# Kernel optimization log

Measured on AMD Instinct MI355X. Metric: run time of the kernel, lower is better.

Reference implementation:

```python
import jax, jax.numpy as jnp
import numpy as np

THRESH = 0.9   # config['thresh_cnn']
R = 2          # config['radius'] -> maxpool kernel 2R+1=5, stride 1, padding R


def setup_inputs() -> dict:
    key = jax.random.key(0)
    # [B=1, C=1, D=64, H=512, W=512]
    pred_vol = jax.random.uniform(key, (1, 1, 64, 512, 512), dtype=jnp.float32)
    return {"pred_vol": pred_vol}


def reference(pred_vol):
    # threshold: keep values > thresh, else 0
    pred_thresh = jnp.where(pred_vol > THRESH, pred_vol, 0.0)
    # 3D max-pool, kernel 2R+1, stride 1, padding R (torch pads with -inf for maxpool)
    k = 2 * R + 1
    mp = jax.lax.reduce_window(
        pred_thresh, -jnp.inf, jax.lax.max,
        window_dimensions=(1, 1, k, k, k),
        window_strides=(1, 1, 1, 1, 1),
        padding=[(0, 0), (0, 0), (R, R), (R, R), (R, R)],
    )
    # keep only strict local maxima of the thresholded volume
    conf_vol = jnp.where((mp > 0.0) & (mp == pred_thresh), mp, 0.0)
    return jnp.squeeze(conf_vol)  # [D, H, W] dense peak confidence map
```

## Files before the change

### kernel.cpp

```cpp
#include <hip/hip_runtime.h>


#define THRESH 0.9f

constexpr int D = 64, H = 512, W = 512;
constexpr int TW = 64;
constexpr int TH = 16;
constexpr int DCHUNK = 8;
constexpr int HALO = 2;
constexpr int LROWS = TH + 2 * HALO;
constexpr int RAWQ  = TW / 4 + 2;
constexpr int RAWQ_S = RAWQ + 1;
constexpr int WMQ   = TW / 4;
constexpr int WMQ_S = WMQ + 1;
constexpr int NS = DCHUNK + 2 * HALO;
constexpr int T_ITERS = NS + 1;

typedef float floatx4 __attribute__((ext_vector_type(4)));

__device__ __forceinline__ float4 thresh4(float4 v) {
    v.x = (v.x > THRESH) ? v.x : 0.f;
    v.y = (v.y > THRESH) ? v.y : 0.f;
    v.z = (v.z > THRESH) ? v.z : 0.f;
    v.w = (v.w > THRESH) ? v.w : 0.f;
    return v;
}

__device__ __forceinline__ float4 max4(float4 a, float4 b) {
    return make_float4(fmaxf(a.x, b.x), fmaxf(a.y, b.y),
                       fmaxf(a.z, b.z), fmaxf(a.w, b.w));
}

__device__ __forceinline__ float4 wmax5(float4 a, float4 b, float4 c) {
    const float f2 = a.z, f3 = a.w, f4 = b.x, f5 = b.y, f6 = b.z, f7 = b.w;
    const float f8 = c.x, f9 = c.y;
    const float m45 = fmaxf(f4, f5);
    const float m56 = fmaxf(f5, f6);
    const float m345 = fmaxf(f3, m45);
    const float m456 = fmaxf(f4, m56);
    const float m567 = fmaxf(m56, f7);
    const float m678 = fmaxf(fmaxf(f6, f7), f8);
    float4 r;
    r.x = fmaxf(fmaxf(f2, f6), m345);
    r.y = fmaxf(fmaxf(f3, f7), m456);
    r.z = fmaxf(fmaxf(f4, f8), m567);
    r.w = fmaxf(fmaxf(f5, f9), m678);
    return r;
}

__global__ __launch_bounds__(256)
void peak3d_kernel(const float* __restrict__ in, float* __restrict__ out) {
    __shared__ float4 raw[2][LROWS * RAWQ_S];
    __shared__ float4 wm [2][LROWS * WMQ_S];

    const int tx = threadIdx.x;
    const int ty = threadIdx.y;
    const int tid = ty * 16 + tx;

    const int w0 = blockIdx.x * TW;
    const int h0 = blockIdx.y * TH;
    const int d0 = blockIdx.z * DCHUNK;

    const int q0 = tid;
    const int q1 = tid + 256;
    const int r0 = q0 / RAWQ, c0 = q0 % RAWQ;
    const int r1 = q1 / RAWQ, c1 = q1 % RAWQ;
    const int lds0 = r0 * RAWQ_S + c0;
    const int lds1 = r1 * RAWQ_S + c1;
    const int gh0 = h0 + r0 - HALO, gw0 = w0 + 4 * c0 - 4;
    const int gh1 = h0 + r1 - HALO, gw1 = w0 + 4 * c1 - 4;
    const bool has1 = (q1 < LROWS * RAWQ);
    const bool ib0 = (gh0 >= 0 && gh0 < H && gw0 >= 0 && gw0 < W);
    const bool ib1 = has1 && (gh1 >= 0 && gh1 < H && gw1 >= 0 && gw1 < W);
    const size_t off0 = ib0 ? ((size_t)gh0 * W + gw0) : 0;
    const size_t off1 = ib1 ? ((size_t)gh1 * W + gw1) : 0;

    const float4 zero4 = make_float4(0.f, 0.f, 0.f, 0.f);
    float4 win[5], cen[5];
#pragma unroll
    for (int k = 0; k < 5; ++k) { win[k] = zero4; cen[k] = zero4; }

    auto loadSlice = [&](int dd, float4& p0, float4& p1) {
        p0 = zero4; p1 = zero4;
        if (dd >= 0 && dd < D) {
            const size_t base = (size_t)dd * (H * W);
            if (ib0) p0 = thresh4(*reinterpret_cast<const float4*>(in + base + off0));
            if (ib1) p1 = thresh4(*reinterpret_cast<const float4*>(in + base + off1));
        }
    };

    float4 p0, p1;
    loadSlice(d0 - HALO, p0, p1);

    for (int jj = 0; jj < (T_ITERS + 4) / 5; ++jj) {
#pragma unroll
        for (int k = 0; k < 5; ++k) {
            const int t = 5 * jj + k;
            if (t < T_ITERS) {
                const int buf = t & 1;

                if (t <= NS - 1) {
                    raw[buf][lds0] = p0;
                    if (has1) raw[buf][lds1] = p1;
                }
                if (t + 1 <= NS - 1) loadSlice(d0 - HALO + t + 1, p0, p1);

                __syncthreads();

                if (t <= NS - 1) {
                    const float4* rp = &raw[buf][ty * RAWQ_S + tx];
                    wm[buf][ty * WMQ_S + tx] = wmax5(rp[0], rp[1], rp[2]);
                    if (tid < (LROWS - TH) * WMQ) {
                        const int r = TH + (tid >> 4), c = tid & 15;
                        const float4* rq = &raw[buf][r * RAWQ_S + c];
                        wm[buf][r * WMQ_S + c] = wmax5(rq[0], rq[1], rq[2]);
                    }
                    cen[k] = raw[buf][(ty + HALO) * RAWQ_S + (tx + 1)];
                }

                if (t >= 1) {
                    const float4* wp = &wm[buf ^ 1][ty * WMQ_S + tx];
                    float4 hv = wp[0];
                    hv = max4(hv, wp[1 * WMQ_S]);
                    hv = max4(hv, wp[2 * WMQ_S]);
                    hv = max4(hv, wp[3 * WMQ_S]);
                    hv = max4(hv, wp[4 * WMQ_S]);
                    win[(k + 4) % 5] = hv;

                    if (t >= 5) {
                        const int dout = d0 + (t - 5);
                        const float4 mp = max4(max4(max4(win[0], win[1]),
                                                    max4(win[2], win[3])), win[4]);
                        const float4 tcc = cen[(k + 2) % 5];
                        floatx4 res;
                        res.x = (mp.x > 0.f && mp.x == tcc.x) ? mp.x : 0.f;
                        res.y = (mp.y > 0.f && mp.y == tcc.y) ? mp.y : 0.f;
                        res.z = (mp.z > 0.f && mp.z == tcc.z) ? mp.z : 0.f;
                        res.w = (mp.w > 0.f && mp.w == tcc.w) ? mp.w : 0.f;
                        floatx4* op = reinterpret_cast<floatx4*>(
                            out + (size_t)dout * (H * W) +
                            (size_t)(h0 + ty) * W + (w0 + 4 * tx));
                        __builtin_nontemporal_store(res, op);
                    }
                }
            }
        }
    }
}

extern "C" void kernel_launch(void* const* d_in, const int* in_sizes, int n_in,
                              void* d_out, int out_size, void* d_ws, size_t ws_size,
                              hipStream_t stream) {
    const float* in = (const float*)d_in[0];
    float* out = (float*)d_out;
    dim3 grid(W / TW, H / TH, D / DCHUNK);
    dim3 block(16, 16, 1);
    hipLaunchKernelGGL(peak3d_kernel, grid, block, 0, stream, in, out);
}
```

Baseline: 122.1 us.

## Prefetch two depth slices ahead and use LDS-only barriers with single-buffered LDS

Restructures the depth-streaming loop so global loads for slice t+2 are issued two iterations ahead in alternating register slots. Replaces __syncthreads with an inline-asm barrier that waits only on LDS counters (lgkmcnt), so outstanding global loads and nontemporal stores are not drained at each barrier. The double-buffered LDS becomes single-buffered, with two barriers per slice and a fully unrolled loop. The aim is to hide memory latency better, at the cost of an extra barrier per iteration and more registers held for prefetch.

```diff
diff --git a/kernel.cpp b/kernel.cpp
--- a/kernel.cpp
+++ b/kernel.cpp
@@ -14,9 +14,12 @@
 constexpr int WMQ   = TW / 4;
 constexpr int WMQ_S = WMQ + 1;
 constexpr int NS = DCHUNK + 2 * HALO;
-constexpr int T_ITERS = NS + 1;
 
 typedef float floatx4 __attribute__((ext_vector_type(4)));
+
+__device__ __forceinline__ void barrier_no_drain() {
+    asm volatile("s_waitcnt lgkmcnt(0)\n\ts_barrier" ::: "memory");
+}
 
 __device__ __forceinline__ float4 thresh4(float4 v) {
     v.x = (v.x > THRESH) ? v.x : 0.f;
@@ -50,8 +53,8 @@
 
 __global__ __launch_bounds__(256)
 void peak3d_kernel(const float* __restrict__ in, float* __restrict__ out) {
-    __shared__ float4 raw[2][LROWS * RAWQ_S];
-    __shared__ float4 wm [2][LROWS * WMQ_S];
+    __shared__ float4 raw[LROWS * RAWQ_S];
+    __shared__ float4 wm [LROWS * WMQ_S];
 
     const int tx = threadIdx.x;
     const int ty = threadIdx.y;
@@ -80,69 +83,65 @@
 #pragma unroll
     for (int k = 0; k < 5; ++k) { win[k] = zero4; cen[k] = zero4; }
 
-    auto loadSlice = [&](int dd, float4& p0, float4& p1) {
-        p0 = zero4; p1 = zero4;
+    auto loadSlice = [&](int dd, float4& a, float4& b) {
+        a = zero4; b = zero4;
         if (dd >= 0 && dd < D) {
             const size_t base = (size_t)dd * (H * W);
-            if (ib0) p0 = thresh4(*reinterpret_cast<const float4*>(in + base + off0));
-            if (ib1) p1 = thresh4(*reinterpret_cast<const float4*>(in + base + off1));
+            if (ib0) a = thresh4(*reinterpret_cast<const float4*>(in + base + off0));
+            if (ib1) b = thresh4(*reinterpret_cast<const float4*>(in + base + off1));
         }
     };
 
-    float4 p0, p1;
-    loadSlice(d0 - HALO, p0, p1);
+    float4 pfa[2], pfb[2];
+    loadSlice(d0 - HALO + 0, pfa[0], pfb[0]);
+    loadSlice(d0 - HALO + 1, pfa[1], pfb[1]);
 
-    for (int jj = 0; jj < (T_ITERS + 4) / 5; ++jj) {
 #pragma unroll
-        for (int k = 0; k < 5; ++k) {
-            const int t = 5 * jj + k;
-            if (t < T_ITERS) {
-                const int buf = t & 1;
+    for (int t = 0; t < NS; ++t) {
+        const int slot = t & 1;
 
-                if (t <= NS - 1) {
-                    raw[buf][lds0] = p0;
-                    if (has1) raw[buf][lds1] = p1;
-                }
-                if (t + 1 <= NS - 1) loadSlice(d0 - HALO + t + 1, p0, p1);
+        raw[lds0] = pfa[slot];
+        if (has1) raw[lds1] = pfb[slot];
+        if (t + 2 < NS) loadSlice(d0 - HALO + t + 2, pfa[slot], pfb[slot]);
 
-                __syncthreads();
+        barrier_no_drain();
 
-                if (t <= NS - 1) {
-                    const float4* rp = &raw[buf][ty * RAWQ_S + tx];
-                    wm[buf][ty * WMQ_S + tx] = wmax5(rp[0], rp[1], rp[2]);
-                    if (tid < (LROWS - TH) * WMQ) {
-                        const int r = TH + (tid >> 4), c = tid & 15;
-                        const float4* rq = &raw[buf][r * RAWQ_S + c];
-                        wm[buf][r * WMQ_S + c] = wmax5(rq[0], rq[1], rq[2]);
-                    }
-                    cen[k] = raw[buf][(ty + HALO) * RAWQ_S + (tx + 1)];
-                }
+        {
+            const float4* rp = &raw[ty * RAWQ_S + tx];
+            wm[ty * WMQ_S + tx] = wmax5(rp[0], rp[1], rp[2]);
+            if (tid < (LROWS - TH) * WMQ) {
+                const int r = TH + (tid >> 4), c = tid & 15;
+                const float4* rq = &raw[r * RAWQ_S + c];
+                wm[r * WMQ_S + c] = wmax5(rq[0], rq[1], rq[2]);
+            }
+            cen[t % 5] = raw[(ty + HALO) * RAWQ_S + (tx + 1)];
+        }
 
-                if (t >= 1) {
-                    const float4* wp = &wm[buf ^ 1][ty * WMQ_S + tx];
-                    float4 hv = wp[0];
-                    hv = max4(hv, wp[1 * WMQ_S]);
-                    hv = max4(hv, wp[2 * WMQ_S]);
-                    hv = max4(hv, wp[3 * WMQ_S]);
-                    hv = max4(hv, wp[4 * WMQ_S]);
-                    win[(k + 4) % 5] = hv;
+        barrier_no_drain();
 
-                    if (t >= 5) {
-                        const int dout = d0 + (t - 5);
-                        const float4 mp = max4(max4(max4(win[0], win[1]),
-                                                    max4(win[2], win[3])), win[4]);
-                        const float4 tcc = cen[(k + 2) % 5];
-                        floatx4 res;
-                        res.x = (mp.x > 0.f && mp.x == tcc.x) ? mp.x : 0.f;
-                        res.y = (mp.y > 0.f && mp.y == tcc.y) ? mp.y : 0.f;
-                        res.z = (mp.z > 0.f && mp.z == tcc.z) ? mp.z : 0.f;
-                        res.w = (mp.w > 0.f && mp.w == tcc.w) ? mp.w : 0.f;
-                        floatx4* op = reinterpret_cast<floatx4*>(
-                            out + (size_t)dout * (H * W) +
-                            (size_t)(h0 + ty) * W + (w0 + 4 * tx));
-                        __builtin_nontemporal_store(res, op);
-                    }
-                }
+        {
+            const float4* wp = &wm[ty * WMQ_S + tx];
+            float4 hv = wp[0];
+            hv = max4(hv, wp[1 * WMQ_S]);
+            hv = max4(hv, wp[2 * WMQ_S]);
+            hv = max4(hv, wp[3 * WMQ_S]);
+            hv = max4(hv, wp[4 * WMQ_S]);
+            win[t % 5] = hv;
+
+            if (t >= 4) {
+                const int dout = d0 + (t - 4);
+                const float4 mp = max4(max4(max4(win[0], win[1]),
+                                            max4(win[2], win[3])), win[4]);
+                const float4 tcc = cen[(t + 3) % 5];
+                floatx4 res;
+                res.x = (mp.x > 0.f && mp.x == tcc.x) ? mp.x : 0.f;
+                res.y = (mp.y > 0.f && mp.y == tcc.y) ? mp.y : 0.f;
+                res.z = (mp.z > 0.f && mp.z == tcc.z) ? mp.z : 0.f;
+                res.w = (mp.w > 0.f && mp.w == tcc.w) ? mp.w : 0.f;
+                floatx4* op = reinterpret_cast<floatx4*>(
+                    out + (size_t)dout * (H * W) +
+                    (size_t)(h0 + ty) * W + (w0 + 4 * tx));
+                __builtin_nontemporal_store(res, op);
             }
         }
     }
```

After: 125.9 us. 3.1% more time.
